# Optimization experiments

Hardware: AMD Instinct MI355X
Metric: run time of the kernel (lower is better)

Reference implementation:

```python
import jax, jax.numpy as jnp
import numpy as np

N_NODES = 50000
N_EDGES = 400000
HID = 128
MSG = 128
N_ROUNDS = 2


def setup_inputs() -> dict:
    key = jax.random.key(0)
    ks = jax.random.split(key, 10)
    s = 0.05
    return {
        "x": jax.random.normal(ks[0], (N_NODES, HID), jnp.float32),
        "h": jax.random.normal(ks[1], (N_NODES, HID), jnp.float32),
        "W_msg": jax.random.normal(ks[2], (MSG, 4 * HID), jnp.float32) * s,
        "b_msg": jax.random.normal(ks[3], (MSG,), jnp.float32) * s,
        "w_ih": jax.random.normal(ks[4], (3 * HID, HID + MSG), jnp.float32) * s,
        "w_hh": jax.random.normal(ks[5], (3 * HID, HID), jnp.float32) * s,
        "b_ih": jax.random.normal(ks[6], (3 * HID,), jnp.float32) * s,
        "b_hh": jax.random.normal(ks[7], (3 * HID,), jnp.float32) * s,
        "src": jax.random.randint(ks[8], (N_EDGES,), 0, N_NODES, jnp.int32),
        "dst": jax.random.randint(ks[9], (N_EDGES,), 0, N_NODES, jnp.int32),
    }


def _gru_cell(inp, h, w_ih, w_hh, b_ih, b_hh):
    # torch.nn.GRUCell math
    gi = inp @ w_ih.T + b_ih   # [N, 3H]
    gh = h @ w_hh.T + b_hh     # [N, 3H]
    i_r, i_z, i_n = jnp.split(gi, 3, axis=1)
    h_r, h_z, h_n = jnp.split(gh, 3, axis=1)
    r = jax.nn.sigmoid(i_r + h_r)
    z = jax.nn.sigmoid(i_z + h_z)
    n = jnp.tanh(i_n + r * h_n)
    return (1.0 - z) * n + z * h


def reference(x, h, W_msg, b_msg, w_ih, w_hh, b_ih, b_hh, src, dst):
    n_nodes = x.shape[0]
    ones_e = jnp.ones((src.shape[0], 1), x.dtype)
    for _ in range(N_ROUNDS):
        hd = jax.lax.stop_gradient(h)  # matches h.detach() in message pass
        # edge gather + concat: [E, 4H]
        feat = jnp.concatenate([x[src], hd[src], x[dst], hd[dst]], axis=1)
        m = feat @ W_msg.T + b_msg  # [E, MSG]
        sums = jax.ops.segment_sum(m, dst, num_segments=n_nodes)
        cnt = jax.ops.segment_sum(ones_e, dst, num_segments=n_nodes)
        c = sums / jnp.maximum(cnt, 1.0)  # mean over mailbox; zeros for deg-0
        h = _gru_cell(jnp.concatenate([x, c], axis=1), h, w_ih, w_hh, b_ih, b_hh)
    return h
```

## Files before the change

kernel.cpp:

```cpp
#include <hip/hip_runtime.h>
#include <hip/hip_bf16.h>

typedef __hip_bfloat16 bf16;
typedef __bf16 bf16x8 __attribute__((ext_vector_type(8)));
typedef float  f32x4  __attribute__((ext_vector_type(4)));

#define N_NODES 50000
#define N_EDGES 400000
#define NT 3125
#define HID 128
#define MSG 128


typedef const __attribute__((address_space(1))) unsigned int* as1_u32p;
typedef __attribute__((address_space(3))) unsigned int* as3_u32p;
__device__ __forceinline__ void gll16(const bf16* g, bf16* l) {
    __builtin_amdgcn_global_load_lds((as1_u32p)(const void*)g,
                                     (as3_u32p)(void*)l, 16, 0, 0);
}

__global__ __launch_bounds__(256)
void gemm_sd_kernel(const bf16* __restrict__ XT,
                    const bf16* __restrict__ HT,
                    const bf16* __restrict__ W,
                    bf16* __restrict__ O, int M) {
    constexpr int K = 256, J = 256;
    __shared__ __align__(16) bf16 Ws[64 * K];

    const int bid = blockIdx.x;
    const int mt  = (bid >> 5) * 8 + (bid & 7);
    const int bnt = (bid >> 3) & 3;
    if (mt * 256 >= M) return;
    const int bm = mt * 256;
    const int bn = bnt * 64;
    const int tid = threadIdx.x;

    const bf16* wsrc = W + (size_t)bnt * 16384;
    #pragma unroll
    for (int i = 0; i < 8; ++i)
        gll16(wsrc + i * 2048 + tid * 8, &Ws[i * 2048 + tid * 8]);
    __syncthreads();

    const int w    = tid >> 6;
    const int lane = tid & 63;
    const int lr   = lane & 15;
    const int kg   = lane >> 4;
    const int mbase = bm + w * 64;

    int tile[4];
    #pragma unroll
    for (int fm = 0; fm < 4; ++fm) {
        int t = (mbase + fm * 16) >> 4;
        tile[fm] = (t < NT) ? t : NT - 1;
    }

    f32x4 acc[4][4] = {};

    #pragma unroll
    for (int k0 = 0; k0 < K; k0 += 32) {
        bf16x8 a[4];
        #pragma unroll
        for (int fm = 0; fm < 4; ++fm) {
            const bf16* ap = (k0 < 128)
                ? XT + ((size_t)tile[fm] * 32 + (k0 >> 3) + kg) * 128 + lr * 8
                : HT + ((size_t)tile[fm] * 16 + ((k0 - 128) >> 3) + kg) * 128 + lr * 8;
            a[fm] = *reinterpret_cast<const bf16x8*>(ap);
        }
        const int kcb = (k0 >> 3) + kg;
        #pragma unroll
        for (int fn = 0; fn < 4; ++fn) {
            bf16x8 b = *reinterpret_cast<const bf16x8*>(
                &Ws[(kcb * 64 + ((fn * 16 + lr) ^ (kcb & 7))) * 8]);
            #pragma unroll
            for (int fm = 0; fm < 4; ++fm)
                acc[fm][fn] = __builtin_amdgcn_mfma_f32_16x16x32_bf16(
                    a[fm], b, acc[fm][fn], 0, 0, 0);
        }
    }

    __syncthreads();
    #pragma unroll
    for (int fn = 0; fn < 4; ++fn) {
        int col = fn * 16 + lr;
        #pragma unroll
        for (int fm = 0; fm < 4; ++fm) {
            int rbase = w * 64 + fm * 16 + kg * 4;
            #pragma unroll
            for (int r = 0; r < 4; ++r) {
                int row = rbase + r;
                int cs = ((((col >> 3) ^ ((row >> 2) & 7))) << 3) | (col & 7);
                Ws[row * 64 + cs] = __float2bfloat16(acc[fm][fn][r]);
            }
        }
    }
    __syncthreads();
    const int colblk = tid & 7;
    const int rbase_o = tid >> 3;
    #pragma unroll
    for (int it = 0; it < 8; ++it) {
        int row = it * 32 + rbase_o;
        int grow = bm + row;
        if (grow < M) {
            int g = (row >> 2) & 7;
            const float4 v = *reinterpret_cast<const float4*>(
                &Ws[row * 64 + ((colblk ^ g) << 3)]);
            *reinterpret_cast<float4*>(O + (size_t)grow * J + bn + colblk * 8) = v;
        }
    }
}

__device__ __forceinline__ float fast_sigmoid(float x) {
    return 1.0f / (1.0f + __expf(-x));
}
__device__ __forceinline__ float fast_tanh(float x) {
    float e = __expf(-2.0f * fabsf(x));
    float t = (1.0f - e) / (1.0f + e);
    return copysignf(t, x);
}

template <int FINAL>
__global__ __launch_bounds__(256, 4)
void gates_kernel(const bf16* __restrict__ XT,
                  const bf16* __restrict__ HT,
                  const bf16* __restrict__ Wg,
                  const float* __restrict__ bg,
                  float* __restrict__ h_out,
                  bf16* __restrict__ HTout,
                  int M) {
    const int bid = blockIdx.x;
    const int mt  = (bid >> 6) * 8 + (bid & 7);
    const int q   = (bid >> 3) & 7;
    if (mt * 256 >= M) return;

    const int tid  = threadIdx.x;
    const int w    = tid >> 6;
    const int lane = tid & 63;
    const int lr   = lane & 15;
    const int kg   = lane >> 4;
    const int mbase = mt * 256 + w * 64;

    int tile[4];
    #pragma unroll
    for (int fm = 0; fm < 4; ++fm) {
        int t = (mbase + fm * 16) >> 4;
        tile[fm] = (t < NT) ? t : NT - 1;
    }
    const bf16* Wb = Wg + ((size_t)kg * 512 + q * 64 + lr) * 8;

    f32x4 acc[4][4] = {};

    #pragma unroll
    for (int ch = 0; ch < 12; ++ch) {
        bf16x8 a[4];
        #pragma unroll
        for (int fm = 0; fm < 4; ++fm) {
            const bf16* ap = (ch < 8)
                ? XT + ((size_t)tile[fm] * 32 + ch * 4 + kg) * 128 + lr * 8
                : HT + ((size_t)tile[fm] * 16 + (ch - 8) * 4 + kg) * 128 + lr * 8;
            a[fm] = *reinterpret_cast<const bf16x8*>(ap);
        }
        #pragma unroll
        for (int gi = 0; gi < 3; ++gi) {
            const int g = (ch < 8) ? gi : ((gi == 2) ? 3 : gi);
            bf16x8 b = *reinterpret_cast<const bf16x8*>(
                Wb + ((size_t)ch * 4 * 512 + g * 16) * 8);
            #pragma unroll
            for (int fm = 0; fm < 4; ++fm)
                acc[fm][g] = __builtin_amdgcn_mfma_f32_16x16x32_bf16(
                    a[fm], b, acc[fm][g], 0, 0, 0);
        }
    }

    const float br  = bg[q * 64 + lr];
    const float bz  = bg[q * 64 + 16 + lr];
    const float bin = bg[q * 64 + 32 + lr];
    const float bhn = bg[q * 64 + 48 + lr];
    const int c = q * 16 + lr;
    #pragma unroll
    for (int fm = 0; fm < 4; ++fm) {
        #pragma unroll
        for (int r = 0; r < 4; ++r) {
            const int row = mbase + fm * 16 + kg * 4 + r;
            if (row >= M) continue;
            float rr = fast_sigmoid(acc[fm][0][r] + br);
            float zz = fast_sigmoid(acc[fm][1][r] + bz);
            float nn = fast_tanh(acc[fm][2][r] + bin +
                                 rr * (acc[fm][3][r] + bhn));
            const size_t hti = ((size_t)(row >> 4) * 16 + (c >> 3)) * 128
                               + (row & 15) * 8 + (c & 7);
            float hin = __bfloat162float(HT[hti]);
            float hv = (1.0f - zz) * nn + zz * hin;
            if (FINAL) {
                h_out[(size_t)row * 128 + c] = hv;
            } else {
                HTout[hti] = __float2bfloat16(hv);
            }
        }
    }
}

#define WSD_N  65536
#define WG_N   196608
__global__ __launch_bounds__(256)
void prep_weights_kernel(const float* __restrict__ W_msg,
                         const float* __restrict__ w_ih,
                         const float* __restrict__ w_hh,
                         const float* __restrict__ b_ih,
                         const float* __restrict__ b_hh,
                         bf16* __restrict__ Wsd,
                         bf16* __restrict__ Wg,
                         float* __restrict__ bg) {
    int gid = blockIdx.x * 256 + threadIdx.x;
    if (gid < WSD_N) {
        int bn_t = gid >> 14;
        int r    = gid & 16383;
        int kc   = r >> 9;
        int r2   = r & 511;
        int js   = r2 >> 3;
        int e    = r2 & 7;
        int jj   = bn_t * 64 + (js ^ (kc & 7));
        int k    = kc * 8 + e;
        float v = (jj < 128) ? W_msg[jj * 512 + k]
                             : W_msg[(jj - 128) * 512 + 256 + k];
        Wsd[gid] = __float2bfloat16(v);
    } else if (gid < WSD_N + WG_N) {
        int i  = gid - WSD_N;
        int kc = i >> 12;
        int j  = (i >> 3) & 511;
        int e  = i & 7;
        int k  = kc * 8 + e;
        int q = j >> 6, g = (j >> 4) & 3, lr = j & 15;
        int c = q * 16 + lr;
        float v;
        if (k < 256) v = (g < 3) ? w_ih[(size_t)(g * 128 + c) * 256 + k] : 0.0f;
        else         v = (g == 2) ? 0.0f
                       : w_hh[(size_t)(((g == 3) ? 2 : g) * 128 + c) * 128 + (k - 256)];
        Wg[i] = __float2bfloat16(v);
    } else if (gid < WSD_N + WG_N + 512) {
        int jp = gid - WSD_N - WG_N;
        int q = jp >> 6, g = (jp >> 4) & 3, lr = jp & 15;
        int c = q * 16 + lr;
        float v;
        if (g == 0)      v = b_ih[c] + b_hh[c];
        else if (g == 1) v = b_ih[128 + c] + b_hh[128 + c];
        else if (g == 2) v = b_ih[256 + c];
        else             v = b_hh[256 + c];
        bg[jp] = v;
    }
}

__global__ __launch_bounds__(256)
void conv_xa_kernel(const float* __restrict__ x, const float* __restrict__ h0,
                    bf16* __restrict__ XT, bf16* __restrict__ HT0, int N) {
    int gid = blockIdx.x * 256 + threadIdx.x;
    if (gid >= N * 32) return;
    const int half = (gid >= N * 16);
    const int i  = half ? gid - N * 16 : gid;
    const int v  = i >> 4;
    const int kc = i & 15;
    const float* src = (half ? h0 : x) + (size_t)v * 128 + kc * 8;
    const float4 f0 = *reinterpret_cast<const float4*>(src);
    const float4 f1 = *reinterpret_cast<const float4*>(src + 4);
    bf16 tmp[8];
    tmp[0] = __float2bfloat16(f0.x); tmp[1] = __float2bfloat16(f0.y);
    tmp[2] = __float2bfloat16(f0.z); tmp[3] = __float2bfloat16(f0.w);
    tmp[4] = __float2bfloat16(f1.x); tmp[5] = __float2bfloat16(f1.y);
    tmp[6] = __float2bfloat16(f1.z); tmp[7] = __float2bfloat16(f1.w);
    bf16* dst = half
        ? HT0 + ((size_t)(v >> 4) * 16 + kc) * 128 + (v & 15) * 8
        : XT  + ((size_t)(v >> 4) * 32 + kc) * 128 + (v & 15) * 8;
    *reinterpret_cast<float4*>(dst) = *reinterpret_cast<const float4*>(tmp);
}

__global__ __launch_bounds__(256)
void deg_kernel(const int* __restrict__ dst, int* __restrict__ cnt, int E) {
    int e = blockIdx.x * 256 + threadIdx.x;
    if (e < E) atomicAdd(&cnt[dst[e]], 1);
}

__global__ __launch_bounds__(256)
void csr_alloc_kernel(const int* __restrict__ cnt, int* __restrict__ off,
                      int* __restrict__ total, int N) {
    int v = blockIdx.x * 256 + threadIdx.x;
    int lane = threadIdx.x & 63;
    int c = (v < N) ? cnt[v] : 0;
    int s = c;
    #pragma unroll
    for (int d = 1; d < 64; d <<= 1) {
        int t = __shfl_up(s, d, 64);
        if (lane >= d) s += t;
    }
    int wave_total = __shfl(s, 63, 64);
    int base = 0;
    if (lane == 63) base = atomicAdd(total, wave_total);
    base = __shfl(base, 63, 64);
    if (v < N) off[v] = base + s - c;
}

__global__ __launch_bounds__(256)
void fill_csr_kernel(const int* __restrict__ src, const int* __restrict__ dst,
                     const int* __restrict__ off, int* __restrict__ cursor,
                     int* __restrict__ csr, int E) {
    int e = blockIdx.x * 256 + threadIdx.x;
    if (e >= E) return;
    int d = dst[e];
    int pos = atomicAdd(&cursor[d], 1);
    csr[off[d] + pos] = src[e];
}

__global__ __launch_bounds__(256)
void agg_kernel(const bf16* __restrict__ SD, const int* __restrict__ csr,
                const int* __restrict__ off, const int* __restrict__ cnt,
                const float* __restrict__ b_msg, bf16* __restrict__ XT, int N) {
    const int v    = (blockIdx.x * 256 + threadIdx.x) >> 6;
    const int lane = threadIdx.x & 63;
    if (v >= N) return;
    const int g    = lane >> 4;
    const int sl   = lane & 15;
    const int deg  = cnt[v];
    const int base = off[v];

    float acc[8] = {};
    #pragma unroll 2
    for (int k = g; k < deg; k += 4) {
        int s0 = csr[base + k];
        bf16x8 row = *reinterpret_cast<const bf16x8*>(
            SD + (size_t)s0 * 256 + sl * 8);
        #pragma unroll
        for (int e = 0; e < 8; ++e) acc[e] += (float)row[e];
    }
    #pragma unroll
    for (int e = 0; e < 8; ++e) {
        acc[e] += __shfl_xor(acc[e], 16, 64);
        acc[e] += __shfl_xor(acc[e], 32, 64);
    }

    if (g != 0) return;
    bf16 outb[8];
    if (deg > 0) {
        const float inv = 1.0f / (float)deg;
        bf16x8 d8 = *reinterpret_cast<const bf16x8*>(
            SD + (size_t)v * 256 + 128 + sl * 8);
        const float4 b0 = *reinterpret_cast<const float4*>(b_msg + sl * 8);
        const float4 b1 = *reinterpret_cast<const float4*>(b_msg + sl * 8 + 4);
        const float bm[8] = {b0.x, b0.y, b0.z, b0.w, b1.x, b1.y, b1.z, b1.w};
        #pragma unroll
        for (int e = 0; e < 8; ++e)
            outb[e] = __float2bfloat16(acc[e] * inv + (float)d8[e] + bm[e]);
    } else {
        #pragma unroll
        for (int e = 0; e < 8; ++e) outb[e] = __float2bfloat16(0.0f);
    }
    bf16* dst = XT + ((size_t)(v >> 4) * 32 + 16 + sl) * 128 + (v & 15) * 8;
    *reinterpret_cast<float4*>(dst) = *reinterpret_cast<const float4*>(outb);
}

extern "C" void kernel_launch(void* const* d_in, const int* in_sizes, int n_in,
                              void* d_out, int out_size, void* d_ws, size_t ws_size,
                              hipStream_t stream) {
    const float* x     = (const float*)d_in[0];
    const float* h0    = (const float*)d_in[1];
    const float* W_msg = (const float*)d_in[2];
    const float* b_msg = (const float*)d_in[3];
    const float* w_ih  = (const float*)d_in[4];
    const float* w_hh  = (const float*)d_in[5];
    const float* b_ih  = (const float*)d_in[6];
    const float* b_hh  = (const float*)d_in[7];
    const int*   src   = (const int*)d_in[8];
    const int*   dst   = (const int*)d_in[9];
    float* h = (float*)d_out;

    char* ws = (char*)d_ws;
    size_t off_b = 0;
    auto alloc = [&](size_t bytes) -> void* {
        void* p = ws + off_b;
        off_b = (off_b + bytes + 255) & ~(size_t)255;
        return p;
    };
    int*   meta   = (int*)  alloc(((size_t)2 * N_NODES + 64) * 4);
    int*   cnt    = meta;
    int*   cursor = meta + N_NODES;
    int*   total  = meta + 2 * N_NODES;
    int*   off    = (int*)  alloc((size_t)N_NODES * 4);
    int*   csr    = (int*)  alloc((size_t)N_EDGES * 4);
    bf16*  Wsd_b  = (bf16*) alloc((size_t)WSD_N * 2);
    bf16*  Wg_b   = (bf16*) alloc((size_t)WG_N * 2);
    float* bg     = (float*)alloc(512 * 4);
    bf16*  XT     = (bf16*) alloc((size_t)NT * 32 * 128 * 2);
    bf16*  HT0    = (bf16*) alloc((size_t)NT * 16 * 128 * 2);
    bf16*  HT1    = (bf16*) alloc((size_t)NT * 16 * 128 * 2);
    bf16*  SD     = (bf16*) alloc((size_t)N_NODES * 256 * 2);

    hipMemsetAsync(meta, 0, ((size_t)2 * N_NODES + 64) * 4, stream);
    deg_kernel<<<(N_EDGES + 255) / 256, 256, 0, stream>>>(dst, cnt, N_EDGES);
    csr_alloc_kernel<<<(N_NODES + 255) / 256, 256, 0, stream>>>(cnt, off, total, N_NODES);
    fill_csr_kernel<<<(N_EDGES + 255) / 256, 256, 0, stream>>>(src, dst, off, cursor,
                                                               csr, N_EDGES);
    prep_weights_kernel<<<(WSD_N + WG_N + 512 + 255) / 256, 256, 0, stream>>>(
        W_msg, w_ih, w_hh, b_ih, b_hh, Wsd_b, Wg_b, bg);
    conv_xa_kernel<<<(N_NODES * 32 + 255) / 256, 256, 0, stream>>>(
        x, h0, XT, HT0, N_NODES);

    const int SD_GRID    = 25 * 32;
    const int GATES_GRID = 25 * 64;
    const int AGG_GRID   = (N_NODES * 64 + 255) / 256;

    gemm_sd_kernel<<<SD_GRID, 256, 0, stream>>>(XT, HT0, Wsd_b, SD, N_NODES);
    agg_kernel<<<AGG_GRID, 256, 0, stream>>>(
        SD, csr, off, cnt, b_msg, XT, N_NODES);
    gates_kernel<0><<<GATES_GRID, 256, 0, stream>>>(
        XT, HT0, Wg_b, bg, nullptr, HT1, N_NODES);

    gemm_sd_kernel<<<SD_GRID, 256, 0, stream>>>(XT, HT1, Wsd_b, SD, N_NODES);
    agg_kernel<<<AGG_GRID, 256, 0, stream>>>(
        SD, csr, off, cnt, b_msg, XT, N_NODES);
    gates_kernel<1><<<GATES_GRID, 256, 0, stream>>>(
        XT, HT1, Wg_b, bg, h, nullptr, N_NODES);
}
```

Before: 223.7 us.

## Fuse setup kernels, drop LDS weight staging in SD GEMM, add MFMA priority

Merges the degree-count, weight-prep and input-conversion kernels into one setup launch to cut launch count and serialization. The SD GEMM now reads weights straight from global memory in an unswizzled layout instead of staging them in LDS, which removes a barrier and the LDS fill. s_setprio is placed around the MFMA loops in both GEMMs. The trade-off is more global or L2 traffic for the B operand and a changed Wsd layout that must match the new indexing.

```diff
diff --git a/kernel.cpp b/kernel.cpp
--- a/kernel.cpp
+++ b/kernel.cpp
@@ -11,13 +11,6 @@
 #define HID 128
 #define MSG 128
 
-
-typedef const __attribute__((address_space(1))) unsigned int* as1_u32p;
-typedef __attribute__((address_space(3))) unsigned int* as3_u32p;
-__device__ __forceinline__ void gll16(const bf16* g, bf16* l) {
-    __builtin_amdgcn_global_load_lds((as1_u32p)(const void*)g,
-                                     (as3_u32p)(void*)l, 16, 0, 0);
-}
 
 __global__ __launch_bounds__(256)
 void gemm_sd_kernel(const bf16* __restrict__ XT,
@@ -25,7 +18,7 @@
                     const bf16* __restrict__ W,
                     bf16* __restrict__ O, int M) {
     constexpr int K = 256, J = 256;
-    __shared__ __align__(16) bf16 Ws[64 * K];
+    __shared__ __align__(16) bf16 Cs[256 * 64];
 
     const int bid = blockIdx.x;
     const int mt  = (bid >> 5) * 8 + (bid & 7);
@@ -35,12 +28,6 @@
     const int bn = bnt * 64;
     const int tid = threadIdx.x;
 
-    const bf16* wsrc = W + (size_t)bnt * 16384;
-    #pragma unroll
-    for (int i = 0; i < 8; ++i)
-        gll16(wsrc + i * 2048 + tid * 8, &Ws[i * 2048 + tid * 8]);
-    __syncthreads();
-
     const int w    = tid >> 6;
     const int lane = tid & 63;
     const int lr   = lane & 15;
@@ -53,6 +40,7 @@
         int t = (mbase + fm * 16) >> 4;
         tile[fm] = (t < NT) ? t : NT - 1;
     }
+    const bf16* Wb = W + ((size_t)kg * 256 + bn + lr) * 8;
 
     f32x4 acc[4][4] = {};
 
@@ -66,19 +54,19 @@
                 : HT + ((size_t)tile[fm] * 16 + ((k0 - 128) >> 3) + kg) * 128 + lr * 8;
             a[fm] = *reinterpret_cast<const bf16x8*>(ap);
         }
-        const int kcb = (k0 >> 3) + kg;
+        __builtin_amdgcn_s_setprio(1);
         #pragma unroll
         for (int fn = 0; fn < 4; ++fn) {
             bf16x8 b = *reinterpret_cast<const bf16x8*>(
-                &Ws[(kcb * 64 + ((fn * 16 + lr) ^ (kcb & 7))) * 8]);
+                Wb + (((size_t)(k0 >> 3)) * 256 + fn * 16) * 8);
             #pragma unroll
             for (int fm = 0; fm < 4; ++fm)
                 acc[fm][fn] = __builtin_amdgcn_mfma_f32_16x16x32_bf16(
                     a[fm], b, acc[fm][fn], 0, 0, 0);
         }
-    }
-
-    __syncthreads();
+        __builtin_amdgcn_s_setprio(0);
+    }
+
     #pragma unroll
     for (int fn = 0; fn < 4; ++fn) {
         int col = fn * 16 + lr;
@@ -89,7 +77,7 @@
             for (int r = 0; r < 4; ++r) {
                 int row = rbase + r;
                 int cs = ((((col >> 3) ^ ((row >> 2) & 7))) << 3) | (col & 7);
-                Ws[row * 64 + cs] = __float2bfloat16(acc[fm][fn][r]);
+                Cs[row * 64 + cs] = __float2bfloat16(acc[fm][fn][r]);
             }
         }
     }
@@ -103,7 +91,7 @@
         if (grow < M) {
             int g = (row >> 2) & 7;
             const float4 v = *reinterpret_cast<const float4*>(
-                &Ws[row * 64 + ((colblk ^ g) << 3)]);
+                &Cs[row * 64 + ((colblk ^ g) << 3)]);
             *reinterpret_cast<float4*>(O + (size_t)grow * J + bn + colblk * 8) = v;
         }
     }
@@ -159,6 +147,7 @@
                 : HT + ((size_t)tile[fm] * 16 + (ch - 8) * 4 + kg) * 128 + lr * 8;
             a[fm] = *reinterpret_cast<const bf16x8*>(ap);
         }
+        __builtin_amdgcn_s_setprio(1);
         #pragma unroll
         for (int gi = 0; gi < 3; ++gi) {
             const int g = (ch < 8) ? gi : ((gi == 2) ? 3 : gi);
@@ -169,6 +158,7 @@
                 acc[fm][g] = __builtin_amdgcn_mfma_f32_16x16x32_bf16(
                     a[fm], b, acc[fm][g], 0, 0, 0);
         }
+        __builtin_amdgcn_s_setprio(0);
     }
 
     const float br  = bg[q * 64 + lr];
@@ -201,61 +191,63 @@
 
 #define WSD_N  65536
 #define WG_N   196608
+#define PREP_N (WSD_N + WG_N + 512)
 __global__ __launch_bounds__(256)
-void prep_weights_kernel(const float* __restrict__ W_msg,
-                         const float* __restrict__ w_ih,
-                         const float* __restrict__ w_hh,
-                         const float* __restrict__ b_ih,
-                         const float* __restrict__ b_hh,
-                         bf16* __restrict__ Wsd,
-                         bf16* __restrict__ Wg,
-                         float* __restrict__ bg) {
+void setup_kernel(const int* __restrict__ dst, int* __restrict__ cnt,
+                  const float* __restrict__ W_msg,
+                  const float* __restrict__ w_ih,
+                  const float* __restrict__ w_hh,
+                  const float* __restrict__ b_ih,
+                  const float* __restrict__ b_hh,
+                  bf16* __restrict__ Wsd, bf16* __restrict__ Wg,
+                  float* __restrict__ bg,
+                  const float* __restrict__ x, const float* __restrict__ h0,
+                  bf16* __restrict__ XT, bf16* __restrict__ HT0) {
     int gid = blockIdx.x * 256 + threadIdx.x;
-    if (gid < WSD_N) {
-        int bn_t = gid >> 14;
-        int r    = gid & 16383;
-        int kc   = r >> 9;
-        int r2   = r & 511;
-        int js   = r2 >> 3;
-        int e    = r2 & 7;
-        int jj   = bn_t * 64 + (js ^ (kc & 7));
-        int k    = kc * 8 + e;
-        float v = (jj < 128) ? W_msg[jj * 512 + k]
-                             : W_msg[(jj - 128) * 512 + 256 + k];
-        Wsd[gid] = __float2bfloat16(v);
-    } else if (gid < WSD_N + WG_N) {
-        int i  = gid - WSD_N;
-        int kc = i >> 12;
-        int j  = (i >> 3) & 511;
-        int e  = i & 7;
-        int k  = kc * 8 + e;
-        int q = j >> 6, g = (j >> 4) & 3, lr = j & 15;
-        int c = q * 16 + lr;
-        float v;
-        if (k < 256) v = (g < 3) ? w_ih[(size_t)(g * 128 + c) * 256 + k] : 0.0f;
-        else         v = (g == 2) ? 0.0f
-                       : w_hh[(size_t)(((g == 3) ? 2 : g) * 128 + c) * 128 + (k - 256)];
-        Wg[i] = __float2bfloat16(v);
-    } else if (gid < WSD_N + WG_N + 512) {
-        int jp = gid - WSD_N - WG_N;
-        int q = jp >> 6, g = (jp >> 4) & 3, lr = jp & 15;
-        int c = q * 16 + lr;
-        float v;
-        if (g == 0)      v = b_ih[c] + b_hh[c];
-        else if (g == 1) v = b_ih[128 + c] + b_hh[128 + c];
-        else if (g == 2) v = b_ih[256 + c];
-        else             v = b_hh[256 + c];
-        bg[jp] = v;
-    }
-}
-
-__global__ __launch_bounds__(256)
-void conv_xa_kernel(const float* __restrict__ x, const float* __restrict__ h0,
-                    bf16* __restrict__ XT, bf16* __restrict__ HT0, int N) {
-    int gid = blockIdx.x * 256 + threadIdx.x;
-    if (gid >= N * 32) return;
-    const int half = (gid >= N * 16);
-    const int i  = half ? gid - N * 16 : gid;
+    if (gid < N_EDGES) {
+        atomicAdd(&cnt[dst[gid]], 1);
+        return;
+    }
+    gid -= N_EDGES;
+    if (gid < PREP_N) {
+        if (gid < WSD_N) {
+            int kc = gid >> 11;
+            int j  = (gid >> 3) & 255;
+            int e  = gid & 7;
+            int k  = kc * 8 + e;
+            float v = (j < 128) ? W_msg[(size_t)j * 512 + k]
+                                : W_msg[(size_t)(j - 128) * 512 + 256 + k];
+            Wsd[gid] = __float2bfloat16(v);
+        } else if (gid < WSD_N + WG_N) {
+            int i  = gid - WSD_N;
+            int kc = i >> 12;
+            int j  = (i >> 3) & 511;
+            int e  = i & 7;
+            int k  = kc * 8 + e;
+            int q = j >> 6, g = (j >> 4) & 3, lr = j & 15;
+            int c = q * 16 + lr;
+            float v;
+            if (k < 256) v = (g < 3) ? w_ih[(size_t)(g * 128 + c) * 256 + k] : 0.0f;
+            else         v = (g == 2) ? 0.0f
+                           : w_hh[(size_t)(((g == 3) ? 2 : g) * 128 + c) * 128 + (k - 256)];
+            Wg[i] = __float2bfloat16(v);
+        } else {
+            int jp = gid - WSD_N - WG_N;
+            int q = jp >> 6, g = (jp >> 4) & 3, lr = jp & 15;
+            int c = q * 16 + lr;
+            float v;
+            if (g == 0)      v = b_ih[c] + b_hh[c];
+            else if (g == 1) v = b_ih[128 + c] + b_hh[128 + c];
+            else if (g == 2) v = b_ih[256 + c];
+            else             v = b_hh[256 + c];
+            bg[jp] = v;
+        }
+        return;
+    }
+    gid -= PREP_N;
+    if (gid >= N_NODES * 32) return;
+    const int half = (gid >= N_NODES * 16);
+    const int i  = half ? gid - N_NODES * 16 : gid;
     const int v  = i >> 4;
     const int kc = i & 15;
     const float* src = (half ? h0 : x) + (size_t)v * 128 + kc * 8;
@@ -266,16 +258,10 @@
     tmp[2] = __float2bfloat16(f0.z); tmp[3] = __float2bfloat16(f0.w);
     tmp[4] = __float2bfloat16(f1.x); tmp[5] = __float2bfloat16(f1.y);
     tmp[6] = __float2bfloat16(f1.z); tmp[7] = __float2bfloat16(f1.w);
-    bf16* dst = half
+    bf16* dstp = half
         ? HT0 + ((size_t)(v >> 4) * 16 + kc) * 128 + (v & 15) * 8
         : XT  + ((size_t)(v >> 4) * 32 + kc) * 128 + (v & 15) * 8;
-    *reinterpret_cast<float4*>(dst) = *reinterpret_cast<const float4*>(tmp);
-}
-
-__global__ __launch_bounds__(256)
-void deg_kernel(const int* __restrict__ dst, int* __restrict__ cnt, int E) {
-    int e = blockIdx.x * 256 + threadIdx.x;
-    if (e < E) atomicAdd(&cnt[dst[e]], 1);
+    *reinterpret_cast<float4*>(dstp) = *reinterpret_cast<const float4*>(tmp);
 }
 
 __global__ __launch_bounds__(256)
@@ -392,14 +378,13 @@
     bf16*  SD     = (bf16*) alloc((size_t)N_NODES * 256 * 2);
 
     hipMemsetAsync(meta, 0, ((size_t)2 * N_NODES + 64) * 4, stream);
-    deg_kernel<<<(N_EDGES + 255) / 256, 256, 0, stream>>>(dst, cnt, N_EDGES);
+    const int SETUP_N = N_EDGES + PREP_N + N_NODES * 32;
+    setup_kernel<<<(SETUP_N + 255) / 256, 256, 0, stream>>>(
+        dst, cnt, W_msg, w_ih, w_hh, b_ih, b_hh, Wsd_b, Wg_b, bg,
+        x, h0, XT, HT0);
     csr_alloc_kernel<<<(N_NODES + 255) / 256, 256, 0, stream>>>(cnt, off, total, N_NODES);
     fill_csr_kernel<<<(N_EDGES + 255) / 256, 256, 0, stream>>>(src, dst, off, cursor,
                                                                csr, N_EDGES);
-    prep_weights_kernel<<<(WSD_N + WG_N + 512 + 255) / 256, 256, 0, stream>>>(
-        W_msg, w_ih, w_hh, b_ih, b_hh, Wsd_b, Wg_b, bg);
-    conv_xa_kernel<<<(N_NODES * 32 + 255) / 256, 256, 0, stream>>>(
-        x, h0, XT, HT0, N_NODES);
 
     const int SD_GRID    = 25 * 32;
     const int GATES_GRID = 25 * 64;
```

Measured after the change: 215.4 us. 1.04x faster.
